# Kernel optimization log

Hardware: AMD Instinct MI355X
Metric: run time of the kernel (lower is better)

The kernel has to match this reference:

```python
import jax, jax.numpy as jnp
import numpy as np

PATCH_SIZE = 16


def setup_inputs() -> dict:
    key = jax.random.key(0)
    images = jax.random.normal(key, (64, 384, 384, 3), dtype=jnp.float32)
    return {"images": images}


def reference(images) -> jnp.ndarray:
    # images: [B, H, W, 3], channels-last. Extract non-overlapping PxP patches
    # and flatten each (row-major over (P, P, 3), matching torch.flatten).
    b, h, w, c = images.shape
    p = PATCH_SIZE
    g = h // p  # grid size
    # [B, G, P, G, P, C] -> [B, G, G, P, P, C] -> [B, G*G, P*P*C]
    x = images.reshape(b, g, p, g, p, c)
    x = x.transpose(0, 1, 3, 2, 4, 5)
    return x.reshape(b, g * g, p * p * c)
```

## Files before the change

kernel.cpp:

```cpp
#include <hip/hip_runtime.h>


typedef float f4 __attribute__((ext_vector_type(4)));

constexpr int C     = 3;
constexpr int P     = 16;
constexpr int G     = 24;
constexpr int ROW4  = 384 * C / 4;
constexpr int IMG4  = 384 * ROW4;
constexpr int HR    = 8;
constexpr int TILE4 = HR * ROW4;
constexpr int LSTR  = ROW4 + 1;
constexpr int BLOCK = 256;
constexpr int PT    = TILE4 / BLOCK;
constexpr int NSLAB = 64 * G * 2;

constexpr int GY4   = G * P * P * C / 4;
constexpr int HALF4 = HR * P * C / 4;

__global__ __launch_bounds__(BLOCK)
void patches_kernel(const f4* __restrict__ in, f4* __restrict__ out) {
    __shared__ f4 lds[HR * LSTR];

    const int s    = blockIdx.x;
    const int half = s & 1;
    const int bg   = s >> 1;
    const int gy   = bg % G;
    const int b    = bg / G;
    const int t    = threadIdx.x;

    const int in_base  = b * IMG4 + (gy * P + half * HR) * ROW4;
    const int out_base = b * IMG4 + gy * GY4 + half * HALF4;

    f4 v[PT];
#pragma unroll
    for (int j = 0; j < PT; ++j)
        v[j] = __builtin_nontemporal_load(in + in_base + t + j * BLOCK);

#pragma unroll
    for (int j = 0; j < PT; ++j) {
        int i   = t + j * BLOCK;
        int row = i / ROW4;
        int col = i - row * ROW4;
        lds[row * LSTR + col] = v[j];
    }
    __syncthreads();

#pragma unroll
    for (int j = 0; j < PT; ++j) {
        int o  = t + j * BLOCK;
        int gx = o / 96;
        int w  = o - gx * 96;
        int py = w / 12;
        int k  = w - py * 12;
        f4 u = lds[py * LSTR + gx * 12 + k];
        __builtin_nontemporal_store(u, out + out_base + gx * 192 + w);
    }
}

extern "C" void kernel_launch(void* const* d_in, const int* in_sizes, int n_in,
                              void* d_out, int out_size, void* d_ws, size_t ws_size,
                              hipStream_t stream) {
    const f4* in  = (const f4*)d_in[0];
    f4*       out = (f4*)d_out;
    patches_kernel<<<NSLAB, BLOCK, 0, stream>>>(in, out);
}
```

Before: 186.0 us.

## Use persistent blocks with register double-buffered prefetch of the next slab

Launches a fixed grid of 1024 blocks, each handling three slabs in a loop. The next slab's global loads are issued into a second register buffer before the current slab is staged through LDS and stored, so load latency overlaps with the transpose and stores. The cost is doubled register use (PT=9 f4 per buffer) and fewer blocks in flight for the GPU to hide latency, and the manual barriers and waitcnt need to be correct.

```diff
diff --git a/kernel.cpp b/kernel.cpp
--- a/kernel.cpp
+++ b/kernel.cpp
@@ -14,47 +14,76 @@
 constexpr int BLOCK = 256;
 constexpr int PT    = TILE4 / BLOCK;
 constexpr int NSLAB = 64 * G * 2;
+constexpr int GRID  = 1024;
+constexpr int NITER = NSLAB / GRID;
 
 constexpr int GY4   = G * P * P * C / 4;
 constexpr int HALF4 = HR * P * C / 4;
 
-__global__ __launch_bounds__(BLOCK)
+__device__ __forceinline__ int in_base_of(int s) {
+    int half = s & 1, bg = s >> 1;
+    int gy = bg % G, b = bg / G;
+    return b * IMG4 + (gy * P + half * HR) * ROW4;
+}
+__device__ __forceinline__ int out_base_of(int s) {
+    int half = s & 1, bg = s >> 1;
+    int gy = bg % G, b = bg / G;
+    return b * IMG4 + gy * GY4 + half * HALF4;
+}
+
+__global__ __launch_bounds__(BLOCK, 4)
 void patches_kernel(const f4* __restrict__ in, f4* __restrict__ out) {
     __shared__ f4 lds[HR * LSTR];
+    const int t  = threadIdx.x;
+    const int s0 = blockIdx.x;
 
-    const int s    = blockIdx.x;
-    const int half = s & 1;
-    const int bg   = s >> 1;
-    const int gy   = bg % G;
-    const int b    = bg / G;
-    const int t    = threadIdx.x;
-
-    const int in_base  = b * IMG4 + (gy * P + half * HR) * ROW4;
-    const int out_base = b * IMG4 + gy * GY4 + half * HALF4;
-
-    f4 v[PT];
+    f4 v[PT], u[PT];
+    {
+        const f4* p = in + in_base_of(s0) + t;
 #pragma unroll
-    for (int j = 0; j < PT; ++j)
-        v[j] = __builtin_nontemporal_load(in + in_base + t + j * BLOCK);
+        for (int j = 0; j < PT; ++j)
+            v[j] = __builtin_nontemporal_load(p + j * BLOCK);
+    }
 
 #pragma unroll
-    for (int j = 0; j < PT; ++j) {
-        int i   = t + j * BLOCK;
-        int row = i / ROW4;
-        int col = i - row * ROW4;
-        lds[row * LSTR + col] = v[j];
-    }
-    __syncthreads();
+    for (int i = 0; i < NITER; ++i) {
+        if (i + 1 < NITER) {
+            const f4* p = in + in_base_of(s0 + (i + 1) * GRID) + t;
+#pragma unroll
+            for (int j = 0; j < PT; ++j)
+                u[j] = __builtin_nontemporal_load(p + j * BLOCK);
+            __builtin_amdgcn_sched_barrier(0);
+        }
+
+        if (i > 0)
+            __builtin_amdgcn_s_barrier();
 
 #pragma unroll
-    for (int j = 0; j < PT; ++j) {
-        int o  = t + j * BLOCK;
-        int gx = o / 96;
-        int w  = o - gx * 96;
-        int py = w / 12;
-        int k  = w - py * 12;
-        f4 u = lds[py * LSTR + gx * 12 + k];
-        __builtin_nontemporal_store(u, out + out_base + gx * 192 + w);
+        for (int j = 0; j < PT; ++j) {
+            int idx = t + j * BLOCK;
+            int row = idx / ROW4;
+            int col = idx - row * ROW4;
+            lds[row * LSTR + col] = v[j];
+        }
+        asm volatile("s_waitcnt lgkmcnt(0)" ::: "memory");
+        __builtin_amdgcn_s_barrier();
+
+        const int ob = out_base_of(s0 + i * GRID);
+#pragma unroll
+        for (int j = 0; j < PT; ++j) {
+            int o  = t + j * BLOCK;
+            int gx = o / 96;
+            int w  = o - gx * 96;
+            int py = w / 12;
+            int k  = w - py * 12;
+            f4 x = lds[py * LSTR + gx * 12 + k];
+            __builtin_nontemporal_store(x, out + ob + gx * 192 + w);
+        }
+
+        if (i + 1 < NITER) {
+#pragma unroll
+            for (int j = 0; j < PT; ++j) v[j] = u[j];
+        }
     }
 }
 
@@ -63,5 +92,5 @@
                               hipStream_t stream) {
     const f4* in  = (const f4*)d_in[0];
     f4*       out = (f4*)d_out;
-    patches_kernel<<<NSLAB, BLOCK, 0, stream>>>(in, out);
+    patches_kernel<<<GRID, BLOCK, 0, stream>>>(in, out);
 }
```

Result: no change. 185.5 us (median of 2 runs) (-0.3%).
